# Kernel tuning notes

Hardware: AMD Instinct MI355X
Metric: run time of the kernel (lower is better)

Reference implementation:

```python
import math
import jax, jax.numpy as jnp
import numpy as np

D = 512        # encoder_dim
LLM = 4096     # llm_dim
H = 8          # heads
L = 2          # depth
FF = 4 * D     # feedforward hidden
DH = D // H    # head dim
EPS = 1e-5


def setup_inputs() -> dict:
    key = jax.random.key(0)
    ks = jax.random.split(key, 16)
    s_d = 1.0 / math.sqrt(D)
    s_ff = 1.0 / math.sqrt(FF)
    inp = {
        "x": jax.random.normal(ks[0], (1, 8192, D), dtype=jnp.float32),
        # per-layer params, leading dim L
        "ln1_g": jnp.ones((L, D), jnp.float32),
        "ln1_b": jnp.zeros((L, D), jnp.float32),
        "Wq": jax.random.normal(ks[1], (L, D, D), jnp.float32) * s_d,
        "Wk": jax.random.normal(ks[2], (L, D, D), jnp.float32) * s_d,
        "Wv": jax.random.normal(ks[3], (L, D, D), jnp.float32) * s_d,
        "Wo": jax.random.normal(ks[4], (L, D, D), jnp.float32) * s_d,
        "bo": jnp.zeros((L, D), jnp.float32),
        "ln2_g": jnp.ones((L, D), jnp.float32),
        "ln2_b": jnp.zeros((L, D), jnp.float32),
        "W1": jax.random.normal(ks[5], (L, D, FF), jnp.float32) * s_d,
        "b1": jnp.zeros((L, FF), jnp.float32),
        "W2": jax.random.normal(ks[6], (L, FF, D), jnp.float32) * s_ff,
        "b2": jnp.zeros((L, D), jnp.float32),
        # final projector (xavier-like)
        "proj_W": jax.random.normal(ks[7], (D, LLM), jnp.float32) * math.sqrt(2.0 / (D + LLM)),
        "proj_b": jnp.zeros((LLM,), jnp.float32),
    }
    return inp


def _layernorm(h, g, b):
    mu = jnp.mean(h, axis=-1, keepdims=True)
    var = jnp.var(h, axis=-1, keepdims=True)
    return (h - mu) * jax.lax.rsqrt(var + EPS) * g + b


def _sinusoidal_pe(n, d):
    pos = jnp.arange(n, dtype=jnp.float32)[:, None]
    div = jnp.exp(jnp.arange(0, d, 2, dtype=jnp.float32) * (-math.log(10000.0) / d))
    pe = jnp.zeros((n, d), jnp.float32)
    pe = pe.at[:, 0::2].set(jnp.sin(pos * div))
    pe = pe.at[:, 1::2].set(jnp.cos(pos * div))
    return pe


def reference(x, ln1_g, ln1_b, Wq, Wk, Wv, Wo, bo, ln2_g, ln2_b, W1, b1, W2, b2, proj_W, proj_b):
    B, N, _ = x.shape
    x = x + _sinusoidal_pe(N, D)[None]  # positional encoding (dropout = identity at eval)
    scale = DH ** -0.5
    for l in range(L):
        # --- linear self-attention block (PreNorm + residual) ---
        h = _layernorm(x, ln1_g[l], ln1_b[l])
        q = (h @ Wq[l]).reshape(B, N, H, DH).transpose(0, 2, 1, 3)  # bhnd
        k = (h @ Wk[l]).reshape(B, N, H, DH).transpose(0, 2, 1, 3)
        v = (h @ Wv[l]).reshape(B, N, H, DH).transpose(0, 2, 1, 3)
        q = jax.nn.softmax(q, axis=-1) * scale        # softmax over feature dim
        k = jax.nn.softmax(k, axis=-2)                # softmax over sequence dim
        ctx = jnp.einsum('bhnd,bhne->bhde', k, v)     # small [B,H,DH,DH] context
        o = jnp.einsum('bhnd,bhde->bhne', q, ctx)
        o = o.transpose(0, 2, 1, 3).reshape(B, N, D)
        x = x + (o @ Wo[l] + bo[l])
        # --- feedforward block (PreNorm + residual, exact GELU) ---
        h = _layernorm(x, ln2_g[l], ln2_b[l])
        x = x + (jax.nn.gelu(h @ W1[l] + b1[l], approximate=False) @ W2[l] + b2[l])
    x = jnp.squeeze(x, 0)  # batch==1, matches torch x.squeeze(0)
    return x @ proj_W + proj_b  # [N, LLM]
```

## Files before the change

kernel.cpp:

```cpp
#include <hip/hip_runtime.h>
#include <hip/hip_bf16.h>
#include <math.h>

constexpr int N_SEQ = 8192;
constexpr int D     = 512;
constexpr int NH    = 8;
constexpr int FFDIM = 2048;
constexpr int LLMD  = 4096;
constexpr int NLAYER= 2;

typedef __bf16 bf16x8 __attribute__((ext_vector_type(8)));
typedef float  f32x4  __attribute__((ext_vector_type(4)));
typedef unsigned short u16x8 __attribute__((ext_vector_type(8)));

__device__ __forceinline__ unsigned short f2bf(float x) {
  unsigned u = __builtin_bit_cast(unsigned, x);
  unsigned r = (u + 0x7FFFu + ((u >> 16) & 1u)) >> 16;
  return (unsigned short)r;
}
__device__ __forceinline__ float bf2f(unsigned short u) {
  unsigned x = ((unsigned)u) << 16;
  return __builtin_bit_cast(float, x);
}

#define GLOAD16(g, l)                                                        \
  __builtin_amdgcn_global_load_lds(                                          \
      (const __attribute__((address_space(1))) void*)(g),                    \
      (__attribute__((address_space(3))) void*)(l), 16, 0, 0)

__global__ __launch_bounds__(256) void prep_kernel(const float* __restrict__ Wq,
                                                   const float* __restrict__ Wk,
                                                   const float* __restrict__ Wv,
                                                   const float* __restrict__ Wo,
                                                   const float* __restrict__ W1,
                                                   const float* __restrict__ W2,
                                                   const float* __restrict__ Wp,
                                                   unsigned short* __restrict__ WT,
                                                   const float* __restrict__ xin,
                                                   float* __restrict__ X,
                                                   unsigned short* __restrict__ Hb,
                                                   const float* __restrict__ g,
                                                   const float* __restrict__ b) {
  int bid = blockIdx.x;
  if (bid >= 8192) {
    int row  = ((bid - 8192) * 256 + (int)threadIdx.x) >> 6;
    int lane = threadIdx.x & 63;
    const float* p = xin + (size_t)row * D + lane * 8;
    float x[8];
#pragma unroll
    for (int i = 0; i < 8; ++i) {
      int d = lane * 8 + i;
      float freq = __expf((float)(d & ~1) * (-9.210340371976184f / 512.0f));
      float arg = (float)row * freq;
      float pe = (d & 1) ? cosf(arg) : sinf(arg);
      x[i] = p[i] + pe;
    }
    float s = 0.f, sq = 0.f;
#pragma unroll
    for (int i = 0; i < 8; ++i) { s += x[i]; sq += x[i] * x[i]; }
#pragma unroll
    for (int o = 32; o > 0; o >>= 1) { s += __shfl_xor(s, o); sq += __shfl_xor(sq, o); }
    float mu  = s * (1.0f / D);
    float var = sq * (1.0f / D) - mu * mu;
    float rs  = rsqrtf(var + 1e-5f);
    float* Xp = X + (size_t)row * D + lane * 8;
    u16x8 r;
#pragma unroll
    for (int i = 0; i < 8; ++i) {
      Xp[i] = x[i];
      r[i] = f2bf((x[i] - mu) * rs * g[lane * 8 + i] + b[lane * 8 + i]);
    }
    *(u16x8*)(Hb + (size_t)row * D + lane * 8) = r;
    return;
  }
  const float* src; unsigned short* dst; int K, N, tile;
  if (bid < 2048) {
    int mat = bid >> 8; int w = mat >> 1, l = mat & 1;
    const float* s4 = (w == 0) ? Wq : (w == 1) ? Wk : (w == 2) ? Wv : Wo;
    src = s4 + (size_t)l * 262144;
    dst = WT + ((size_t)l * 4 + w) * 262144;
    K = 512; N = 512; tile = bid & 255;
  } else if (bid < 4096) {
    int b2 = bid - 2048; int l = b2 >> 10;
    src = W1 + (size_t)l * 1048576; dst = WT + 2097152 + (size_t)l * 1048576;
    K = 512; N = 2048; tile = b2 & 1023;
  } else if (bid < 6144) {
    int b2 = bid - 4096; int l = b2 >> 10;
    src = W2 + (size_t)l * 1048576; dst = WT + 4194304 + (size_t)l * 1048576;
    K = 2048; N = 512; tile = b2 & 1023;
  } else {
    src = Wp; dst = WT + 6291456; K = 512; N = 4096; tile = bid - 6144;
  }
  int tilesN = N >> 5;
  int bk = (tile / tilesN) << 5, bn = (tile % tilesN) << 5;
  __shared__ float s[32][33];
  int r = threadIdx.x >> 5, c = threadIdx.x & 31;
#pragma unroll
  for (int i = 0; i < 4; ++i)
    s[r + 8 * i][c] = src[(size_t)(bk + r + 8 * i) * N + bn + c];
  __syncthreads();
#pragma unroll
  for (int i = 0; i < 4; ++i) {
    int rr = r + 8 * i;
    dst[(size_t)(bn + rr) * K + bk + c] = f2bf(s[c][rr]);
  }
}

__global__ __launch_bounds__(256) void ln_bf16(const float* __restrict__ in,
                                               unsigned short* __restrict__ out,
                                               const float* __restrict__ g,
                                               const float* __restrict__ b) {
  int row  = (blockIdx.x * 256 + threadIdx.x) >> 6;
  int lane = threadIdx.x & 63;
  const float* p = in + (size_t)row * D + lane * 8;
  f32x4 v0 = *(const f32x4*)p;
  f32x4 v1 = *(const f32x4*)(p + 4);
  float s  = v0[0] + v0[1] + v0[2] + v0[3] + v1[0] + v1[1] + v1[2] + v1[3];
  float sq = v0[0]*v0[0] + v0[1]*v0[1] + v0[2]*v0[2] + v0[3]*v0[3]
           + v1[0]*v1[0] + v1[1]*v1[1] + v1[2]*v1[2] + v1[3]*v1[3];
#pragma unroll
  for (int o = 32; o > 0; o >>= 1) { s += __shfl_xor(s, o); sq += __shfl_xor(sq, o); }
  float mu  = s * (1.0f / D);
  float var = sq * (1.0f / D) - mu * mu;
  float rs  = rsqrtf(var + 1e-5f);
  f32x4 g0 = *(const f32x4*)(g + lane * 8);
  f32x4 g1 = *(const f32x4*)(g + lane * 8 + 4);
  f32x4 b0 = *(const f32x4*)(b + lane * 8);
  f32x4 b1 = *(const f32x4*)(b + lane * 8 + 4);
  u16x8 r;
#pragma unroll
  for (int i = 0; i < 4; ++i) r[i]     = f2bf((v0[i] - mu) * rs * g0[i] + b0[i]);
#pragma unroll
  for (int i = 0; i < 4; ++i) r[i + 4] = f2bf((v1[i] - mu) * rs * g1[i] + b1[i]);
  *(u16x8*)(out + (size_t)row * D + lane * 8) = r;
}

template <int FLAGS, int BN>
__global__ __launch_bounds__(256) void mgemm2(const unsigned short* __restrict__ A,
                                              const unsigned short* __restrict__ Bt,
                                              const float* __restrict__ bias,
                                              const float* __restrict__ res,
                                              float* __restrict__ C,
                                              unsigned short* __restrict__ Cb,
                                              int M, int N, int K) {
  constexpr int WNI = BN / 32;
  __shared__ unsigned short As[4][128][32];
  __shared__ unsigned short Bs[4][BN][32];
  const int tid = threadIdx.x;
  const int lane = tid & 63, wv = tid >> 6;
  const int bm = blockIdx.y * 128, bn = blockIdx.x * BN;
  const int wr = (wv >> 1) * 64, wc = (wv & 1) * (BN / 2);
  f32x4 acc[4][WNI] = {};

  const int srA = wv * 32 + (lane >> 2);
  const int sc  = (lane & 3) * 8;
  const unsigned short* Ap0 = A + (size_t)(bm + srA) * K + sc;
  const unsigned short* Ap1 = Ap0 + (size_t)16 * K;
  const int srB = wv * (BN / 4) + (lane >> 2);
  const unsigned short* Bp0 = Bt + (size_t)(bn + srB) * K + sc;
  const unsigned short* Bp1 = Bp0 + (size_t)16 * K;
  const int kh = (lane >> 4) * 8;
  const int fr = lane & 15;

  auto stage = [&](int bb, int k0) {
    GLOAD16(Ap0 + k0, &As[bb][srA][sc]);
    GLOAD16(Ap1 + k0, &As[bb][srA + 16][sc]);
    GLOAD16(Bp0 + k0, &Bs[bb][srB][sc]);
    if constexpr (BN == 128) GLOAD16(Bp1 + k0, &Bs[bb][srB + 16][sc]);
  };

  const int nt = K >> 5;
  stage(0, 0);
  stage(1, 32);
  stage(2, 64);
  for (int t = 0; t < nt; ++t) {
    __builtin_amdgcn_sched_barrier(0);
    if constexpr (BN == 128)
      asm volatile("s_waitcnt vmcnt(8)" ::: "memory");
    else
      asm volatile("s_waitcnt vmcnt(6)" ::: "memory");
    __builtin_amdgcn_s_barrier();
    __builtin_amdgcn_sched_barrier(0);
    const int bb = t & 3;
    bf16x8 af[4], bfv[WNI];
#pragma unroll
    for (int mi = 0; mi < 4; ++mi)
      af[mi] = *(const bf16x8*)&As[bb][wr + mi * 16 + fr][kh];
#pragma unroll
    for (int ni = 0; ni < WNI; ++ni)
      bfv[ni] = *(const bf16x8*)&Bs[bb][wc + ni * 16 + fr][kh];
    if (t + 3 < nt) stage((t + 3) & 3, (t + 3) << 5);
#pragma unroll
    for (int mi = 0; mi < 4; ++mi)
#pragma unroll
      for (int ni = 0; ni < WNI; ++ni)
        acc[mi][ni] = __builtin_amdgcn_mfma_f32_16x16x32_bf16(af[mi], bfv[ni], acc[mi][ni], 0, 0, 0);
  }

  const int r4 = (lane >> 4) * 4, cc = lane & 15;
#pragma unroll
  for (int mi = 0; mi < 4; ++mi) {
#pragma unroll
    for (int ni = 0; ni < WNI; ++ni) {
      int col = bn + wc + ni * 16 + cc;
      float bsv = (FLAGS & 1) ? bias[col] : 0.0f;
      f32x4 v = acc[mi][ni];
#pragma unroll
      for (int j = 0; j < 4; ++j) {
        int row = bm + wr + mi * 16 + r4 + j;
        float x = v[j] + bsv;
        if (FLAGS & 2) x = 0.5f * x * (1.0f + erff(x * 0.7071067811865475f));
        if (FLAGS & 4) x += res[(size_t)row * N + col];
        if (!(FLAGS & 16)) C[(size_t)row * N + col] = x;
        if (FLAGS & 8) Cb[(size_t)row * N + col] = f2bf(x);
      }
    }
  }
}

__global__ __launch_bounds__(256) void qkv_gemm(const unsigned short* __restrict__ A,
                                                const unsigned short* __restrict__ Bt,
                                                unsigned short* __restrict__ Qb,
                                                unsigned short* __restrict__ Kb,
                                                unsigned short* __restrict__ Vb,
                                                float* __restrict__ pm,
                                                float* __restrict__ ps) {
  constexpr int K = 512;
  __shared__ unsigned short As[4][128][32];
  __shared__ unsigned short Bs[4][128][32];
  const int tid = threadIdx.x;
  const int lane = tid & 63, wv = tid >> 6;
  const int bm = blockIdx.y * 128, bn = blockIdx.x * 128;
  const int wr = (wv >> 1) * 64, wc = (wv & 1) * 64;
  f32x4 acc[4][4] = {};

  const int srA = wv * 32 + (lane >> 2);
  const int sc  = (lane & 3) * 8;
  const unsigned short* Ap0 = A + (size_t)(bm + srA) * K + sc;
  const unsigned short* Ap1 = Ap0 + (size_t)16 * K;
  const unsigned short* Bp0 = Bt + (size_t)(bn + srA) * K + sc;
  const unsigned short* Bp1 = Bp0 + (size_t)16 * K;
  const int kh = (lane >> 4) * 8;
  const int fr = lane & 15;

  auto stage = [&](int bb, int k0) {
    GLOAD16(Ap0 + k0, &As[bb][srA][sc]);
    GLOAD16(Ap1 + k0, &As[bb][srA + 16][sc]);
    GLOAD16(Bp0 + k0, &Bs[bb][srA][sc]);
    GLOAD16(Bp1 + k0, &Bs[bb][srA + 16][sc]);
  };

  stage(0, 0);
  stage(1, 32);
  stage(2, 64);
  for (int t = 0; t < 16; ++t) {
    __builtin_amdgcn_sched_barrier(0);
    asm volatile("s_waitcnt vmcnt(8)" ::: "memory");
    __builtin_amdgcn_s_barrier();
    __builtin_amdgcn_sched_barrier(0);
    const int bb = t & 3;
    bf16x8 af[4], bfv[4];
#pragma unroll
    for (int mi = 0; mi < 4; ++mi)
      af[mi] = *(const bf16x8*)&As[bb][wr + mi * 16 + fr][kh];
#pragma unroll
    for (int ni = 0; ni < 4; ++ni)
      bfv[ni] = *(const bf16x8*)&Bs[bb][wc + ni * 16 + fr][kh];
    if (t + 3 < 16) stage((t + 3) & 3, (t + 3) << 5);
#pragma unroll
    for (int mi = 0; mi < 4; ++mi)
#pragma unroll
      for (int ni = 0; ni < 4; ++ni)
        acc[mi][ni] = __builtin_amdgcn_mfma_f32_16x16x32_bf16(af[mi], bfv[ni], acc[mi][ni], 0, 0, 0);
  }

  const int r4 = (lane >> 4) * 4, cc = lane & 15;
  if (bn < 512) {
#pragma unroll
    for (int mi = 0; mi < 4; ++mi) {
#pragma unroll
      for (int j = 0; j < 4; ++j) {
        float v0 = acc[mi][0][j], v1 = acc[mi][1][j];
        float v2 = acc[mi][2][j], v3 = acc[mi][3][j];
        float m = fmaxf(fmaxf(v0, v1), fmaxf(v2, v3));
        m = fmaxf(m, __shfl_xor(m, 1)); m = fmaxf(m, __shfl_xor(m, 2));
        m = fmaxf(m, __shfl_xor(m, 4)); m = fmaxf(m, __shfl_xor(m, 8));
        float e0 = __expf(v0 - m), e1 = __expf(v1 - m);
        float e2 = __expf(v2 - m), e3 = __expf(v3 - m);
        float s = e0 + e1 + e2 + e3;
        s += __shfl_xor(s, 1); s += __shfl_xor(s, 2);
        s += __shfl_xor(s, 4); s += __shfl_xor(s, 8);
        float w = 0.125f / s;
        int row = bm + wr + mi * 16 + r4 + j;
        unsigned short* qr = Qb + (size_t)row * 512 + bn + wc + cc;
        qr[0] = f2bf(e0 * w); qr[16] = f2bf(e1 * w);
        qr[32] = f2bf(e2 * w); qr[48] = f2bf(e3 * w);
      }
    }
  } else if (bn < 1024) {
    int colb = bn - 512 + wc + cc;
    int prow = blockIdx.y * 2 + (wr ? 1 : 0);
#pragma unroll
    for (int ni = 0; ni < 4; ++ni) {
      float kf[4][4];
      float m = -1e30f;
#pragma unroll
      for (int mi = 0; mi < 4; ++mi)
#pragma unroll
        for (int j = 0; j < 4; ++j) {
          unsigned short kr = f2bf(acc[mi][ni][j]);
          Kb[(size_t)(bm + wr + mi * 16 + r4 + j) * 512 + colb + ni * 16] = kr;
          kf[mi][j] = bf2f(kr);
          m = fmaxf(m, kf[mi][j]);
        }
      m = fmaxf(m, __shfl_xor(m, 16));
      m = fmaxf(m, __shfl_xor(m, 32));
      float s = 0.f;
#pragma unroll
      for (int mi = 0; mi < 4; ++mi)
#pragma unroll
        for (int j = 0; j < 4; ++j) s += __expf(kf[mi][j] - m);
      s += __shfl_xor(s, 16);
      s += __shfl_xor(s, 32);
      if (lane < 16) {
        pm[(size_t)prow * 512 + colb + ni * 16] = m;
        ps[(size_t)prow * 512 + colb + ni * 16] = s;
      }
    }
  } else {
    int colv = bn - 1024 + wc + cc;
#pragma unroll
    for (int mi = 0; mi < 4; ++mi)
#pragma unroll
      for (int ni = 0; ni < 4; ++ni) {
        f32x4 v = acc[mi][ni];
#pragma unroll
        for (int j = 0; j < 4; ++j)
          Vb[(size_t)(bm + wr + mi * 16 + r4 + j) * 512 + colv + ni * 16] = f2bf(v[j]);
      }
  }
}

__global__ __launch_bounds__(256) void ctx_kernel(const unsigned short* __restrict__ kb,
                                                  const unsigned short* __restrict__ vb,
                                                  const float* __restrict__ pm,
                                                  const float* __restrict__ ps,
                                                  float* __restrict__ part) {
  int chunk = blockIdx.x, h = blockIdx.y, t = threadIdx.x;
  __shared__ float ks[64][64], vs[64][64];
  __shared__ float qm[4][64], qsum[4][64], scm[64], sci[64];
  {
    int c = t & 63, qt = t >> 6;
    float m = -1e30f, s = 0.f;
    for (int r = qt * 32; r < qt * 32 + 32; ++r) {
      float vm = pm[(size_t)r * 512 + h * 64 + c];
      float vp = ps[(size_t)r * 512 + h * 64 + c];
      float nm = fmaxf(m, vm);
      s = s * __expf(m - nm) + vp * __expf(vm - nm);
      m = nm;
    }
    qm[qt][c] = m; qsum[qt][c] = s;
  }
  __syncthreads();
  if (t < 64) {
    float M = fmaxf(fmaxf(qm[0][t], qm[1][t]), fmaxf(qm[2][t], qm[3][t]));
    float S = qsum[0][t] * __expf(qm[0][t] - M) + qsum[1][t] * __expf(qm[1][t] - M)
            + qsum[2][t] * __expf(qm[2][t] - M) + qsum[3][t] * __expf(qm[3][t] - M);
    scm[t] = M; sci[t] = 1.0f / S;
  }
  float acc[16] = {};
  int e0 = (t >> 6) * 16, dd = t & 63;
  for (int s0 = 0; s0 < 256; s0 += 64) {
    size_t rowbase = (size_t)chunk * 256 + s0;
    __syncthreads();
    for (int i = t; i < 1024; i += 256) {
      int r = i >> 4, c4 = (i & 15) * 4;
      ushort4 k4 = *(const ushort4*)&kb[(rowbase + r) * 512 + h * 64 + c4];
      ks[r][c4 + 0] = __expf(bf2f(k4.x) - scm[c4 + 0]) * sci[c4 + 0];
      ks[r][c4 + 1] = __expf(bf2f(k4.y) - scm[c4 + 1]) * sci[c4 + 1];
      ks[r][c4 + 2] = __expf(bf2f(k4.z) - scm[c4 + 2]) * sci[c4 + 2];
      ks[r][c4 + 3] = __expf(bf2f(k4.w) - scm[c4 + 3]) * sci[c4 + 3];
      ushort4 v4 = *(const ushort4*)&vb[(rowbase + r) * 512 + h * 64 + c4];
      vs[r][c4 + 0] = bf2f(v4.x); vs[r][c4 + 1] = bf2f(v4.y);
      vs[r][c4 + 2] = bf2f(v4.z); vs[r][c4 + 3] = bf2f(v4.w);
    }
    __syncthreads();
    for (int r = 0; r < 64; ++r) {
      float kd = ks[r][dd];
      float4 v0 = *(const float4*)&vs[r][e0];
      float4 v1 = *(const float4*)&vs[r][e0 + 4];
      float4 v2 = *(const float4*)&vs[r][e0 + 8];
      float4 v3 = *(const float4*)&vs[r][e0 + 12];
      acc[0]  = fmaf(kd, v0.x, acc[0]);  acc[1]  = fmaf(kd, v0.y, acc[1]);
      acc[2]  = fmaf(kd, v0.z, acc[2]);  acc[3]  = fmaf(kd, v0.w, acc[3]);
      acc[4]  = fmaf(kd, v1.x, acc[4]);  acc[5]  = fmaf(kd, v1.y, acc[5]);
      acc[6]  = fmaf(kd, v1.z, acc[6]);  acc[7]  = fmaf(kd, v1.w, acc[7]);
      acc[8]  = fmaf(kd, v2.x, acc[8]);  acc[9]  = fmaf(kd, v2.y, acc[9]);
      acc[10] = fmaf(kd, v2.z, acc[10]); acc[11] = fmaf(kd, v2.w, acc[11]);
      acc[12] = fmaf(kd, v3.x, acc[12]); acc[13] = fmaf(kd, v3.y, acc[13]);
      acc[14] = fmaf(kd, v3.z, acc[14]); acc[15] = fmaf(kd, v3.w, acc[15]);
    }
  }
  float* pb = &part[((size_t)h * 32 + chunk) * 4096 + dd * 64 + e0];
#pragma unroll
  for (int j = 0; j < 16; ++j) pb[j] = acc[j];
}

__global__ __launch_bounds__(256) void ctx_reduce_kernel(const float* __restrict__ part,
                                                         float* __restrict__ ctx) {
  int idx = blockIdx.x * 256 + threadIdx.x;
  int h = idx >> 12, de = idx & 4095;
  float s = 0.f;
#pragma unroll 8
  for (int c = 0; c < 32; ++c) s += part[((size_t)h * 32 + c) * 4096 + de];
  ctx[(size_t)h * 4096 + de] = s;
}

__global__ __launch_bounds__(256) void ctxw2_kernel(const float* __restrict__ ctx,
                                                    const float* __restrict__ Wo,
                                                    unsigned short* __restrict__ WPT) {
  int ct = blockIdx.x, h = blockIdx.y, t = threadIdx.x;
  __shared__ float cs[64][64];
  __shared__ float wo[64][64];
  for (int i = t; i < 4096; i += 256) {
    cs[i >> 6][i & 63] = ctx[(size_t)h * 4096 + i];
    wo[i >> 6][i & 63] = Wo[(size_t)(h * 64 + (i >> 6)) * 512 + ct * 64 + (i & 63)];
  }
  __syncthreads();
  int cl = t & 63, dg = (t >> 6) * 16;
  float accv[16];
#pragma unroll
  for (int j = 0; j < 16; ++j) accv[j] = 0.f;
  for (int e = 0; e < 64; ++e) {
    float w = wo[e][cl];
#pragma unroll
    for (int j = 0; j < 16; ++j) accv[j] = fmaf(cs[dg + j][e], w, accv[j]);
  }
  u16x8 o0, o1;
#pragma unroll
  for (int j = 0; j < 8; ++j) { o0[j] = f2bf(accv[j]); o1[j] = f2bf(accv[j + 8]); }
  unsigned short* dst = WPT + (size_t)(ct * 64 + cl) * 512 + h * 64 + dg;
  *(u16x8*)dst = o0;
  *(u16x8*)(dst + 8) = o1;
}

extern "C" void kernel_launch(void* const* d_in, const int* in_sizes, int n_in,
                              void* d_out, int out_size, void* d_ws, size_t ws_size,
                              hipStream_t stream) {
  const float* x_in  = (const float*)d_in[0];
  const float* ln1_g = (const float*)d_in[1];
  const float* ln1_b = (const float*)d_in[2];
  const float* Wq    = (const float*)d_in[3];
  const float* Wk    = (const float*)d_in[4];
  const float* Wv    = (const float*)d_in[5];
  const float* Wo    = (const float*)d_in[6];
  const float* bo    = (const float*)d_in[7];
  const float* ln2_g = (const float*)d_in[8];
  const float* ln2_b = (const float*)d_in[9];
  const float* W1    = (const float*)d_in[10];
  const float* b1    = (const float*)d_in[11];
  const float* W2    = (const float*)d_in[12];
  const float* b2    = (const float*)d_in[13];
  const float* projW = (const float*)d_in[14];
  const float* projb = (const float*)d_in[15];
  float* out = (float*)d_out;
  float* ws  = (float*)d_ws;
  constexpr size_t M1 = 1u << 20;

  float* X    = ws;
  float* CTXP = ws + 4 * M1;
  float* PM   = ws + 5 * M1;
  float* PS   = PM + 65536;
  float* CTX  = PS + 65536;
  unsigned short* Qb  = (unsigned short*)(ws + 6 * M1);
  unsigned short* Kb  = (unsigned short*)(ws + 8 * M1);
  unsigned short* Vb  = (unsigned short*)(ws + 10 * M1);
  unsigned short* Hb  = (unsigned short*)(ws + 12 * M1);
  unsigned short* Xb  = (unsigned short*)(ws + 14 * M1);
  unsigned short* FFH = (unsigned short*)(ws + 16 * M1);
  unsigned short* WT  = (unsigned short*)(ws + 24 * M1);
  unsigned short* WPT = (unsigned short*)(ws + 28 * M1);

  prep_kernel<<<10240, 256, 0, stream>>>(Wq, Wk, Wv, Wo, W1, W2, projW, WT,
                                         x_in, X, Hb, ln1_g, ln1_b);

  dim3 gqkv(1536 / 128, N_SEQ / 128);
  dim3 g512n(512 / 64, N_SEQ / 128);
  dim3 gff1(FFDIM / 128, N_SEQ / 128);
  dim3 gproj(LLMD / 128, N_SEQ / 128);

  for (int l = 0; l < NLAYER; ++l) {
    const unsigned short* WQKV = WT + (size_t)l * 1048576;
    const unsigned short* W1T  = WT + 2097152 + (size_t)l * 1048576;
    const unsigned short* W2T  = WT + 4194304 + (size_t)l * 1048576;

    qkv_gemm<<<gqkv, 256, 0, stream>>>(Hb, WQKV, Qb, Kb, Vb, PM, PS);
    ctx_kernel<<<dim3(32, NH), 256, 0, stream>>>(Kb, Vb, PM, PS, CTXP);
    ctx_reduce_kernel<<<128, 256, 0, stream>>>(CTXP, CTX);
    ctxw2_kernel<<<dim3(8, NH), 256, 0, stream>>>(CTX, Wo + (size_t)l * D * D, WPT);
    mgemm2<5, 64><<<g512n, 256, 0, stream>>>(Qb, WPT, bo + l * D, X, X, nullptr,
                                             N_SEQ, 512, 512);
    ln_bf16<<<N_SEQ / 4, 256, 0, stream>>>(X, Hb, ln2_g + l * D, ln2_b + l * D);
    mgemm2<27, 128><<<gff1, 256, 0, stream>>>(Hb, W1T, b1 + l * FFDIM, nullptr,
                                              nullptr, FFH, N_SEQ, FFDIM, 512);
    if (l == NLAYER - 1) {
      mgemm2<29, 64><<<g512n, 256, 0, stream>>>(FFH, W2T, b2 + l * D, X, nullptr,
                                                Xb, N_SEQ, 512, 2048);
    } else {
      mgemm2<5, 64><<<g512n, 256, 0, stream>>>(FFH, W2T, b2 + l * D, X, X, nullptr,
                                               N_SEQ, 512, 2048);
      ln_bf16<<<N_SEQ / 4, 256, 0, stream>>>(X, Hb, ln1_g + (l + 1) * D,
                                             ln1_b + (l + 1) * D);
    }
  }
  mgemm2<1, 128><<<gproj, 256, 0, stream>>>(Xb, WT + 6291456, projb, nullptr,
                                            out, nullptr, N_SEQ, LLMD, 512);
}
```

Before: 439.5 us.

## Add 256x256 tile GEMM for FF1/projection, fuse ctx reduce, raise MFMA priority

Adds a 512-thread mgemm3 kernel with 256x256 output tiles, used for the FF1 and final projection GEMMs. Larger tiles raise data reuse per byte loaded and halve the grid size in each dimension, at the cost of more registers and shared memory per block and fewer blocks in flight. The separate context-reduction kernel is folded into ctxw2, which removes one launch and one round trip through global memory. s_setprio is raised around the MFMA loops so compute issue is favored over the other waves.

Result: slower. 462.1 us (+5.2%).

```diff
diff --git a/kernel.cpp b/kernel.cpp
--- a/kernel.cpp
+++ b/kernel.cpp
@@ -190,11 +190,13 @@
     for (int ni = 0; ni < WNI; ++ni)
       bfv[ni] = *(const bf16x8*)&Bs[bb][wc + ni * 16 + fr][kh];
     if (t + 3 < nt) stage((t + 3) & 3, (t + 3) << 5);
+    __builtin_amdgcn_s_setprio(1);
 #pragma unroll
     for (int mi = 0; mi < 4; ++mi)
 #pragma unroll
       for (int ni = 0; ni < WNI; ++ni)
         acc[mi][ni] = __builtin_amdgcn_mfma_f32_16x16x32_bf16(af[mi], bfv[ni], acc[mi][ni], 0, 0, 0);
+    __builtin_amdgcn_s_setprio(0);
   }
 
   const int r4 = (lane >> 4) * 4, cc = lane & 15;
@@ -211,6 +213,84 @@
         float x = v[j] + bsv;
         if (FLAGS & 2) x = 0.5f * x * (1.0f + erff(x * 0.7071067811865475f));
         if (FLAGS & 4) x += res[(size_t)row * N + col];
+        if (!(FLAGS & 16)) C[(size_t)row * N + col] = x;
+        if (FLAGS & 8) Cb[(size_t)row * N + col] = f2bf(x);
+      }
+    }
+  }
+}
+
+template <int FLAGS>
+__global__ __launch_bounds__(512, 1) void mgemm3(const unsigned short* __restrict__ A,
+                                                 const unsigned short* __restrict__ Bt,
+                                                 const float* __restrict__ bias,
+                                                 float* __restrict__ C,
+                                                 unsigned short* __restrict__ Cb,
+                                                 int M, int N, int K) {
+  __shared__ unsigned short As[4][256][32];
+  __shared__ unsigned short Bs[4][256][32];
+  const int tid = threadIdx.x;
+  const int lane = tid & 63, wv = tid >> 6;
+  const int bm = blockIdx.y * 256, bn = blockIdx.x * 256;
+  const int wr = (wv >> 2) * 128, wc = (wv & 3) * 64;
+  f32x4 acc[8][4] = {};
+
+  const int srA = wv * 32 + (lane >> 2);
+  const int sc  = (lane & 3) * 8;
+  const unsigned short* Ap0 = A + (size_t)(bm + srA) * K + sc;
+  const unsigned short* Ap1 = Ap0 + (size_t)16 * K;
+  const unsigned short* Bp0 = Bt + (size_t)(bn + srA) * K + sc;
+  const unsigned short* Bp1 = Bp0 + (size_t)16 * K;
+  const int kh = (lane >> 4) * 8;
+  const int fr = lane & 15;
+
+  auto stage = [&](int bb, int k0) {
+    GLOAD16(Ap0 + k0, &As[bb][srA][sc]);
+    GLOAD16(Ap1 + k0, &As[bb][srA + 16][sc]);
+    GLOAD16(Bp0 + k0, &Bs[bb][srA][sc]);
+    GLOAD16(Bp1 + k0, &Bs[bb][srA + 16][sc]);
+  };
+
+  const int nt = K >> 5;
+  stage(0, 0);
+  stage(1, 32);
+  stage(2, 64);
+  for (int t = 0; t < nt; ++t) {
+    __builtin_amdgcn_sched_barrier(0);
+    asm volatile("s_waitcnt vmcnt(8)" ::: "memory");
+    __builtin_amdgcn_s_barrier();
+    __builtin_amdgcn_sched_barrier(0);
+    const int bb = t & 3;
+    bf16x8 af[8], bfv[4];
+#pragma unroll
+    for (int mi = 0; mi < 8; ++mi)
+      af[mi] = *(const bf16x8*)&As[bb][wr + mi * 16 + fr][kh];
+#pragma unroll
+    for (int ni = 0; ni < 4; ++ni)
+      bfv[ni] = *(const bf16x8*)&Bs[bb][wc + ni * 16 + fr][kh];
+    if (t + 3 < nt) stage((t + 3) & 3, (t + 3) << 5);
+    __builtin_amdgcn_s_setprio(1);
+#pragma unroll
+    for (int mi = 0; mi < 8; ++mi)
+#pragma unroll
+      for (int ni = 0; ni < 4; ++ni)
+        acc[mi][ni] = __builtin_amdgcn_mfma_f32_16x16x32_bf16(af[mi], bfv[ni], acc[mi][ni], 0, 0, 0);
+    __builtin_amdgcn_s_setprio(0);
+  }
+
+  const int r4 = (lane >> 4) * 4, cc = lane & 15;
+#pragma unroll
+  for (int mi = 0; mi < 8; ++mi) {
+#pragma unroll
+    for (int ni = 0; ni < 4; ++ni) {
+      int col = bn + wc + ni * 16 + cc;
+      float bsv = (FLAGS & 1) ? bias[col] : 0.0f;
+      f32x4 v = acc[mi][ni];
+#pragma unroll
+      for (int j = 0; j < 4; ++j) {
+        int row = bm + wr + mi * 16 + r4 + j;
+        float x = v[j] + bsv;
+        if (FLAGS & 2) x = 0.5f * x * (1.0f + erff(x * 0.7071067811865475f));
         if (!(FLAGS & 16)) C[(size_t)row * N + col] = x;
         if (FLAGS & 8) Cb[(size_t)row * N + col] = f2bf(x);
       }
@@ -267,11 +347,13 @@
     for (int ni = 0; ni < 4; ++ni)
       bfv[ni] = *(const bf16x8*)&Bs[bb][wc + ni * 16 + fr][kh];
     if (t + 3 < 16) stage((t + 3) & 3, (t + 3) << 5);
+    __builtin_amdgcn_s_setprio(1);
 #pragma unroll
     for (int mi = 0; mi < 4; ++mi)
 #pragma unroll
       for (int ni = 0; ni < 4; ++ni)
         acc[mi][ni] = __builtin_amdgcn_mfma_f32_16x16x32_bf16(af[mi], bfv[ni], acc[mi][ni], 0, 0, 0);
+    __builtin_amdgcn_s_setprio(0);
   }
 
   const int r4 = (lane >> 4) * 4, cc = lane & 15;
@@ -406,24 +488,17 @@
   for (int j = 0; j < 16; ++j) pb[j] = acc[j];
 }
 
-__global__ __launch_bounds__(256) void ctx_reduce_kernel(const float* __restrict__ part,
-                                                         float* __restrict__ ctx) {
-  int idx = blockIdx.x * 256 + threadIdx.x;
-  int h = idx >> 12, de = idx & 4095;
-  float s = 0.f;
-#pragma unroll 8
-  for (int c = 0; c < 32; ++c) s += part[((size_t)h * 32 + c) * 4096 + de];
-  ctx[(size_t)h * 4096 + de] = s;
-}
-
-__global__ __launch_bounds__(256) void ctxw2_kernel(const float* __restrict__ ctx,
+__global__ __launch_bounds__(256) void ctxw2_kernel(const float* __restrict__ ctxp,
                                                     const float* __restrict__ Wo,
                                                     unsigned short* __restrict__ WPT) {
   int ct = blockIdx.x, h = blockIdx.y, t = threadIdx.x;
   __shared__ float cs[64][64];
   __shared__ float wo[64][64];
   for (int i = t; i < 4096; i += 256) {
-    cs[i >> 6][i & 63] = ctx[(size_t)h * 4096 + i];
+    float s = 0.f;
+#pragma unroll 8
+    for (int c = 0; c < 32; ++c) s += ctxp[(((size_t)h * 32 + c) << 12) + i];
+    cs[i >> 6][i & 63] = s;
     wo[i >> 6][i & 63] = Wo[(size_t)(h * 64 + (i >> 6)) * 512 + ct * 64 + (i & 63)];
   }
   __syncthreads();
@@ -471,7 +546,6 @@
   float* CTXP = ws + 4 * M1;
   float* PM   = ws + 5 * M1;
   float* PS   = PM + 65536;
-  float* CTX  = PS + 65536;
   unsigned short* Qb  = (unsigned short*)(ws + 6 * M1);
   unsigned short* Kb  = (unsigned short*)(ws + 8 * M1);
   unsigned short* Vb  = (unsigned short*)(ws + 10 * M1);
@@ -486,8 +560,8 @@
 
   dim3 gqkv(1536 / 128, N_SEQ / 128);
   dim3 g512n(512 / 64, N_SEQ / 128);
-  dim3 gff1(FFDIM / 128, N_SEQ / 128);
-  dim3 gproj(LLMD / 128, N_SEQ / 128);
+  dim3 gff1(FFDIM / 256, N_SEQ / 256);
+  dim3 gproj(LLMD / 256, N_SEQ / 256);
 
   for (int l = 0; l < NLAYER; ++l) {
     const unsigned short* WQKV = WT + (size_t)l * 1048576;
@@ -496,13 +570,12 @@
 
     qkv_gemm<<<gqkv, 256, 0, stream>>>(Hb, WQKV, Qb, Kb, Vb, PM, PS);
     ctx_kernel<<<dim3(32, NH), 256, 0, stream>>>(Kb, Vb, PM, PS, CTXP);
-    ctx_reduce_kernel<<<128, 256, 0, stream>>>(CTXP, CTX);
-    ctxw2_kernel<<<dim3(8, NH), 256, 0, stream>>>(CTX, Wo + (size_t)l * D * D, WPT);
+    ctxw2_kernel<<<dim3(8, NH), 256, 0, stream>>>(CTXP, Wo + (size_t)l * D * D, WPT);
     mgemm2<5, 64><<<g512n, 256, 0, stream>>>(Qb, WPT, bo + l * D, X, X, nullptr,
                                              N_SEQ, 512, 512);
     ln_bf16<<<N_SEQ / 4, 256, 0, stream>>>(X, Hb, ln2_g + l * D, ln2_b + l * D);
-    mgemm2<27, 128><<<gff1, 256, 0, stream>>>(Hb, W1T, b1 + l * FFDIM, nullptr,
-                                              nullptr, FFH, N_SEQ, FFDIM, 512);
+    mgemm3<27><<<gff1, 512, 0, stream>>>(Hb, W1T, b1 + l * FFDIM, nullptr, FFH,
+                                         N_SEQ, FFDIM, 512);
     if (l == NLAYER - 1) {
       mgemm2<29, 64><<<g512n, 256, 0, stream>>>(FFH, W2T, b2 + l * D, X, nullptr,
                                                 Xb, N_SEQ, 512, 2048);
@@ -513,6 +586,6 @@
                                              ln1_b + (l + 1) * D);
     }
   }
-  mgemm2<1, 128><<<gproj, 256, 0, stream>>>(Xb, WT + 6291456, projb, nullptr,
-                                            out, nullptr, N_SEQ, LLMD, 512);
-}
+  mgemm3<1><<<gproj, 512, 0, stream>>>(Xb, WT + 6291456, projb, out, nullptr,
+                                       N_SEQ, LLMD, 512);
+}
```
